# Optimization experiments

Hardware: AMD Instinct MI355X
Metric: run time of the kernel (lower is better)

## Reference

```python
import jax, jax.numpy as jnp
from jax import lax
import numpy as np

TOP_PERCENT = 1.3
KSIZE = 3
SIGMA = 0.3 * ((KSIZE - 1) * 0.5 - 1) + 0.8  # torchvision default sigma for ksize=3 -> 0.8


def _gaussian_kernel1d():
    x = jnp.arange(KSIZE, dtype=jnp.float32) - (KSIZE - 1) / 2.0
    k = jnp.exp(-0.5 * (x / SIGMA) ** 2)
    return k / k.sum()


def setup_inputs() -> dict:
    key = jax.random.key(0)
    img = jax.random.uniform(key, (3, 4096, 4096), dtype=jnp.float32)
    return {"img": img}


def reference(img):
    # --- rgb_to_grayscale (ITU-R 601 coefficients, as torchvision) ---
    gray = 0.2989 * img[0] + 0.587 * img[1] + 0.114 * img[2]  # [H, W]

    # --- separable 3x3 gaussian blur, reflect padding (torchvision) ---
    k = _gaussian_kernel1d()
    p = jnp.pad(gray, 1, mode="reflect")  # [H+2, W+2]
    # horizontal pass
    h = k[0] * p[:, :-2] + k[1] * p[:, 1:-1] + k[2] * p[:, 2:]  # [H+2, W]
    # vertical pass
    blur = k[0] * h[:-2, :] + k[1] * h[1:-1, :] + k[2] * h[2:, :]  # [H, W]

    # --- quantile threshold (linear interpolation, matches torch.quantile) ---
    q = (100.0 - TOP_PERCENT) / 100.0
    threshold = jnp.quantile(blur, q)
    mask = (blur >= threshold).astype(jnp.int32)  # [H, W]

    # --- binary opening with 5x5 ones footprint ---
    # erosion = min filter; outside-image treated as 0 (scipy border_value=0),
    # so pad explicitly with zeros and reduce with VALID windows.
    INT_MAX = np.iinfo(np.int32).max
    INT_MIN = np.iinfo(np.int32).min
    padded = jnp.pad(mask, 2)  # zero pad -> borders erode
    eroded = lax.reduce_window(padded, INT_MAX, lax.min, (5, 5), (1, 1), "VALID")
    # dilation = max filter; identity padding (-inf equiv) matches border_value=0
    opened = lax.reduce_window(eroded, INT_MIN, lax.max, (5, 5), (1, 1), "SAME")

    return opened[None, :, :].astype(jnp.int32)  # [1, H, W]
```

## Files before the change

kernel.cpp:

```cpp
#include <hip/hip_runtime.h>
#include <stdint.h>
#include <cmath>


#define HH 4096
#define WW 4096
#define KRANK 16559111u
#define CAP 65536u

__device__ __forceinline__ unsigned ukey(float v) {
  return (unsigned)(v * 268435456.0f);
}
__device__ __forceinline__ int refl(int i) {
  return i < 0 ? -i : (i > 4095 ? 8190 - i : i);
}
__device__ __forceinline__ float grayf(float r, float g, float b) {
  return __fadd_rn(__fadd_rn(__fmul_rn(0.2989f, r), __fmul_rn(0.587f, g)),
                   __fmul_rn(0.114f, b));
}
__device__ __forceinline__ float tap3(float a, float b, float c, float kn0, float kn1) {
  return __fadd_rn(__fadd_rn(__fmul_rn(kn0, a), __fmul_rn(kn1, b)),
                   __fmul_rn(kn0, c));
}

__global__ __launch_bounds__(256) void k_blur(const float* __restrict__ img,
    float4* __restrict__ blur4, unsigned* __restrict__ hist1,
    float kn0, float kn1) {
  __shared__ unsigned hist[4096];
  const int tid = threadIdx.x;
  for (int i = tid; i < 4096; i += 256) hist[i] = 0u;
  __syncthreads();

  const int lane = tid & 63, wv = tid >> 6;
  const int bc = (blockIdx.x & 15) << 8;
  const int r0 = (blockIdx.x >> 4) << 6;
  const int rstart = r0 + (wv << 4);
  const float* __restrict__ Rp = img;
  const float* __restrict__ Gp = img + 16777216;
  const float* __restrict__ Bp = img + 33554432;
  const int c4 = bc + (lane << 2);

  auto hrow = [&](int r) -> float4 {
    const int gr = refl(r);
    const size_t base = ((size_t)gr << 12) + c4;
    float4 R = *(const float4*)(Rp + base);
    float4 G = *(const float4*)(Gp + base);
    float4 B = *(const float4*)(Bp + base);
    float4 g;
    g.x = grayf(R.x, G.x, B.x);
    g.y = grayf(R.y, G.y, B.y);
    g.z = grayf(R.z, G.z, B.z);
    g.w = grayf(R.w, G.w, B.w);
    float gl = __shfl_up(g.w, 1);
    float gr_ = __shfl_down(g.x, 1);
    if (lane == 0) {
      if (bc == 0) gl = g.y;
      else {
        size_t o = ((size_t)gr << 12) + bc - 1;
        gl = grayf(Rp[o], Gp[o], Bp[o]);
      }
    }
    if (lane == 63) {
      if (bc == 3840) gr_ = g.z;
      else {
        size_t o = ((size_t)gr << 12) + bc + 256;
        gr_ = grayf(Rp[o], Gp[o], Bp[o]);
      }
    }
    float4 h;
    h.x = tap3(gl, g.x, g.y, kn0, kn1);
    h.y = tap3(g.x, g.y, g.z, kn0, kn1);
    h.z = tap3(g.y, g.z, g.w, kn0, kn1);
    h.w = tap3(g.z, g.w, gr_, kn0, kn1);
    return h;
  };

  float4 h0 = hrow(rstart - 1);
  float4 h1 = hrow(rstart);
  for (int i = 0; i < 16; ++i) {
    float4 h2 = hrow(rstart + 1 + i);
    float4 v;
    v.x = tap3(h0.x, h1.x, h2.x, kn0, kn1);
    v.y = tap3(h0.y, h1.y, h2.y, kn0, kn1);
    v.z = tap3(h0.z, h1.z, h2.z, kn0, kn1);
    v.w = tap3(h0.w, h1.w, h2.w, kn0, kn1);
    blur4[(((size_t)(rstart + i) << 12) + c4) >> 2] = v;
    atomicAdd(&hist[ukey(v.x) >> 16], 1u);
    atomicAdd(&hist[ukey(v.y) >> 16], 1u);
    atomicAdd(&hist[ukey(v.z) >> 16], 1u);
    atomicAdd(&hist[ukey(v.w) >> 16], 1u);
    h0 = h1; h1 = h2;
  }
  __syncthreads();
  for (int i = tid; i < 4096; i += 256) {
    unsigned c = hist[i];
    if (c) atomicAdd(&hist1[i], c);
  }
}

__global__ __launch_bounds__(256) void k_sel1(const unsigned* __restrict__ hist1,
                                              unsigned* __restrict__ sel) {
  __shared__ unsigned part[256];
  const int t = threadIdx.x;
  unsigned loc[16];
  unsigned s = 0;
  for (int i = 0; i < 16; ++i) { loc[i] = hist1[t * 16 + i]; s += loc[i]; }
  part[t] = s;
  __syncthreads();
  for (int off = 1; off < 256; off <<= 1) {
    unsigned v = (t >= off) ? part[t - off] : 0u;
    __syncthreads();
    part[t] += v;
    __syncthreads();
  }
  unsigned incl = part[t], excl = incl - s;
  if (excl <= KRANK && KRANK < incl) {
    unsigned p = excl;
    for (int i = 0; i < 16; ++i) {
      if (KRANK < p + loc[i]) { sel[0] = (unsigned)(t * 16 + i); sel[1] = KRANK - p; break; }
      p += loc[i];
    }
  }
}

__global__ __launch_bounds__(256) void k_pass2(const float* __restrict__ blur,
    const unsigned* __restrict__ sel, unsigned* __restrict__ hist2,
    unsigned* __restrict__ cnt, unsigned long long* __restrict__ list,
    unsigned long long* __restrict__ mbits) {
  const unsigned b1 = sel[0];
  const unsigned ub = (b1 + 1u) << 16;
  unsigned i = blockIdx.x * 256 + threadIdx.x;
  unsigned u = ukey(blur[i]);
  unsigned long long w = __ballot(u >= ub);
  if ((threadIdx.x & 63) == 0) mbits[i >> 6] = w;
  if ((u >> 16) == b1) {
    atomicAdd(&hist2[u & 0xFFFFu], 1u);
    unsigned idx = atomicAdd(cnt, 1u);
    if (idx < CAP) list[idx] = ((unsigned long long)i << 16) | (u & 0xFFFFu);
  }
}

__global__ __launch_bounds__(1024) void k_sel2(const unsigned* __restrict__ hist2,
                                               unsigned* __restrict__ sel) {
  __shared__ unsigned part[1024];
  const int t = threadIdx.x;
  const unsigned base = (unsigned)t * 64u;
  unsigned s = 0;
  for (int i = 0; i < 64; ++i) s += hist2[base + i];
  part[t] = s;
  __syncthreads();
  for (int off = 1; off < 1024; off <<= 1) {
    unsigned v = (t >= off) ? part[t - off] : 0u;
    __syncthreads();
    part[t] += v;
    __syncthreads();
  }
  unsigned incl = part[t], excl = incl - s;
  unsigned r1 = sel[1];
  if (excl <= r1 && r1 < incl) {
    unsigned p = excl;
    for (int i = 0; i < 64; ++i) {
      unsigned c = hist2[base + i];
      if (r1 < p + c) { sel[2] = base + i; break; }
      p += c;
    }
  }
}

__global__ __launch_bounds__(256) void k_fixup(
    const unsigned long long* __restrict__ list, const unsigned* __restrict__ cnt,
    const unsigned* __restrict__ sel, unsigned long long* __restrict__ mbits) {
  unsigned n = *cnt; if (n > CAP) n = CAP;
  const unsigned lo = sel[2];
  for (unsigned j = blockIdx.x * 256 + threadIdx.x; j < n; j += 256 * gridDim.x) {
    unsigned long long e = list[j];
    if ((unsigned)(e & 0xFFFFu) >= lo) {
      unsigned long long pix = e >> 16;
      atomicOr(&mbits[pix >> 6], 1ull << (pix & 63));
    }
  }
}

__global__ __launch_bounds__(256) void k_erode(
    const unsigned long long* __restrict__ mbits,
    unsigned long long* __restrict__ ebits) {
  int w = blockIdx.x * 256 + threadIdx.x;
  int r = w >> 6, wc = w & 63;
  unsigned long long acc = ~0ull;
  for (int dr = -2; dr <= 2; ++dr) {
    int rr = r + dr;
    unsigned long long h = 0ull;
    if (rr >= 0 && rr <= HH - 1) {
      int rb = (rr << 6) + wc;
      unsigned long long C = mbits[rb];
      unsigned long long L = (wc > 0) ? mbits[rb - 1] : 0ull;
      unsigned long long R = (wc < 63) ? mbits[rb + 1] : 0ull;
      h = C & ((C >> 1) | (R << 63)) & ((C >> 2) | (R << 62))
            & ((C << 1) | (L >> 63)) & ((C << 2) | (L >> 62));
    }
    acc &= h;
  }
  ebits[w] = acc;
}

__global__ __launch_bounds__(256) void k_dilate_out(
    const unsigned long long* __restrict__ ebits, int4* __restrict__ out4) {
  __shared__ unsigned long long wbuf[256];
  int w = blockIdx.x * 256 + threadIdx.x;
  int r = w >> 6, wc = w & 63;
  unsigned long long acc = 0ull;
  for (int dr = -2; dr <= 2; ++dr) {
    int rr = r + dr;
    if (rr < 0 || rr > HH - 1) continue;
    int rb = (rr << 6) + wc;
    unsigned long long C = ebits[rb];
    unsigned long long L = (wc > 0) ? ebits[rb - 1] : 0ull;
    unsigned long long R = (wc < 63) ? ebits[rb + 1] : 0ull;
    acc |= C | ((C >> 1) | (R << 63)) | ((C >> 2) | (R << 62))
             | ((C << 1) | (L >> 63)) | ((C << 2) | (L >> 62));
  }
  wbuf[threadIdx.x] = acc;
  __syncthreads();
  size_t p0 = (size_t)blockIdx.x * 4096;
  for (int j = threadIdx.x; j < 4096; j += 256) {
    unsigned long long word = wbuf[j >> 4];
    unsigned nib = (unsigned)(word >> ((j & 15) << 2)) & 0xFu;
    out4[p0 + j] = make_int4(nib & 1, (nib >> 1) & 1, (nib >> 2) & 1, (nib >> 3) & 1);
  }
}

extern "C" void kernel_launch(void* const* d_in, const int* in_sizes, int n_in,
                              void* d_out, int out_size, void* d_ws, size_t ws_size,
                              hipStream_t stream) {
  (void)in_sizes; (void)n_in; (void)out_size; (void)ws_size;
  const float* img = (const float*)d_in[0];
  char* ws = (char*)d_ws;

  float* blur = (float*)ws;
  unsigned* hist1 = (unsigned*)(ws + 67108864);
  unsigned* hist2 = (unsigned*)(ws + 67125248);
  unsigned* cnt   = (unsigned*)(ws + 67387392);
  unsigned* sel   = (unsigned*)(ws + 67387456);
  unsigned long long* list  = (unsigned long long*)(ws + 67387520);
  unsigned long long* mbits = (unsigned long long*)(ws + 67911808);
  unsigned long long* ebits = (unsigned long long*)(ws + 70008960);

  float t = 1.0f / 0.8f;
  float k0 = expf(-0.5f * (t * t));
  float k1 = 1.0f;
  float s = (k0 + k1) + k0;
  float kn0 = k0 / s, kn1 = k1 / s;

  hipMemsetAsync(hist1, 0, 16384 + 262144 + 64, stream);
  k_blur<<<1024, 256, 0, stream>>>(img, (float4*)blur, hist1, kn0, kn1);
  k_sel1<<<1, 256, 0, stream>>>(hist1, sel);
  k_pass2<<<65536, 256, 0, stream>>>(blur, sel, hist2, cnt, list, mbits);
  k_sel2<<<1, 1024, 0, stream>>>(hist2, sel);
  k_fixup<<<32, 256, 0, stream>>>(list, cnt, sel, mbits);
  k_erode<<<1024, 256, 0, stream>>>(mbits, ebits);
  k_dilate_out<<<1024, 256, 0, stream>>>(ebits, (int4*)d_out);
}
```

Before: 371.5 us.

## Fuse erode/dilate, merge select with fixup, batch pass2 appends

```diff
diff --git a/kernel.cpp b/kernel.cpp
--- a/kernel.cpp
+++ b/kernel.cpp
@@ -23,50 +23,43 @@
                    __fmul_rn(kn0, c));
 }
 
-__global__ __launch_bounds__(256) void k_blur(const float* __restrict__ img,
+__global__ __launch_bounds__(512) void k_blur(const float* __restrict__ img,
     float4* __restrict__ blur4, unsigned* __restrict__ hist1,
     float kn0, float kn1) {
   __shared__ unsigned hist[4096];
   const int tid = threadIdx.x;
-  for (int i = tid; i < 4096; i += 256) hist[i] = 0u;
+  #pragma unroll
+  for (int i = tid; i < 4096; i += 512) hist[i] = 0u;
   __syncthreads();
 
   const int lane = tid & 63, wv = tid >> 6;
   const int bc = (blockIdx.x & 15) << 8;
   const int r0 = (blockIdx.x >> 4) << 6;
-  const int rstart = r0 + (wv << 4);
+  const int rstart = r0 + (wv << 3);
   const float* __restrict__ Rp = img;
   const float* __restrict__ Gp = img + 16777216;
   const float* __restrict__ Bp = img + 33554432;
   const int c4 = bc + (lane << 2);
+  const int colL = (bc == 0) ? 1 : bc - 1;
+  const int colR = (bc == 3840) ? 4094 : bc + 256;
+  const int hc = (lane == 0) ? colL : ((lane == 63) ? colR : c4);
 
   auto hrow = [&](int r) -> float4 {
-    const int gr = refl(r);
-    const size_t base = ((size_t)gr << 12) + c4;
-    float4 R = *(const float4*)(Rp + base);
-    float4 G = *(const float4*)(Gp + base);
-    float4 B = *(const float4*)(Bp + base);
+    const size_t base = ((size_t)refl(r) << 12);
+    float4 R = *(const float4*)(Rp + base + c4);
+    float4 G = *(const float4*)(Gp + base + c4);
+    float4 B = *(const float4*)(Bp + base + c4);
+    float hr = Rp[base + hc], hg = Gp[base + hc], hb = Bp[base + hc];
     float4 g;
     g.x = grayf(R.x, G.x, B.x);
     g.y = grayf(R.y, G.y, B.y);
     g.z = grayf(R.z, G.z, B.z);
     g.w = grayf(R.w, G.w, B.w);
+    float ghalo = grayf(hr, hg, hb);
     float gl = __shfl_up(g.w, 1);
     float gr_ = __shfl_down(g.x, 1);
-    if (lane == 0) {
-      if (bc == 0) gl = g.y;
-      else {
-        size_t o = ((size_t)gr << 12) + bc - 1;
-        gl = grayf(Rp[o], Gp[o], Bp[o]);
-      }
-    }
-    if (lane == 63) {
-      if (bc == 3840) gr_ = g.z;
-      else {
-        size_t o = ((size_t)gr << 12) + bc + 256;
-        gr_ = grayf(Rp[o], Gp[o], Bp[o]);
-      }
-    }
+    gl = (lane == 0) ? ghalo : gl;
+    gr_ = (lane == 63) ? ghalo : gr_;
     float4 h;
     h.x = tap3(gl, g.x, g.y, kn0, kn1);
     h.y = tap3(g.x, g.y, g.z, kn0, kn1);
@@ -77,7 +70,8 @@
 
   float4 h0 = hrow(rstart - 1);
   float4 h1 = hrow(rstart);
-  for (int i = 0; i < 16; ++i) {
+  #pragma unroll
+  for (int i = 0; i < 8; ++i) {
     float4 h2 = hrow(rstart + 1 + i);
     float4 v;
     v.x = tap3(h0.x, h1.x, h2.x, kn0, kn1);
@@ -92,7 +86,8 @@
     h0 = h1; h1 = h2;
   }
   __syncthreads();
-  for (int i = tid; i < 4096; i += 256) {
+  #pragma unroll
+  for (int i = tid; i < 4096; i += 512) {
     unsigned c = hist[i];
     if (c) atomicAdd(&hist1[i], c);
   }
@@ -127,22 +122,47 @@
     const unsigned* __restrict__ sel, unsigned* __restrict__ hist2,
     unsigned* __restrict__ cnt, unsigned long long* __restrict__ list,
     unsigned long long* __restrict__ mbits) {
+  __shared__ unsigned lcnt, lbase;
+  __shared__ unsigned lidx[256];
+  __shared__ unsigned short lkey[256];
+  if (threadIdx.x == 0) lcnt = 0u;
+  __syncthreads();
   const unsigned b1 = sel[0];
   const unsigned ub = (b1 + 1u) << 16;
-  unsigned i = blockIdx.x * 256 + threadIdx.x;
-  unsigned u = ukey(blur[i]);
-  unsigned long long w = __ballot(u >= ub);
-  if ((threadIdx.x & 63) == 0) mbits[i >> 6] = w;
-  if ((u >> 16) == b1) {
-    atomicAdd(&hist2[u & 0xFFFFu], 1u);
-    unsigned idx = atomicAdd(cnt, 1u);
-    if (idx < CAP) list[idx] = ((unsigned long long)i << 16) | (u & 0xFFFFu);
-  }
-}
-
-__global__ __launch_bounds__(1024) void k_sel2(const unsigned* __restrict__ hist2,
-                                               unsigned* __restrict__ sel) {
+  const unsigned base = blockIdx.x * 8192u + threadIdx.x;
+  #pragma unroll 4
+  for (int it = 0; it < 32; ++it) {
+    unsigned i = base + (unsigned)it * 256u;
+    unsigned u = ukey(blur[i]);
+    unsigned long long w = __ballot(u >= ub);
+    if ((threadIdx.x & 63) == 0) mbits[i >> 6] = w;
+    if ((u >> 16) == b1) {
+      atomicAdd(&hist2[u & 0xFFFFu], 1u);
+      unsigned x = atomicAdd(&lcnt, 1u);
+      if (x < 256u) { lidx[x] = i; lkey[x] = (unsigned short)(u & 0xFFFFu); }
+      else {
+        unsigned g = atomicAdd(cnt, 1u);
+        if (g < CAP) list[g] = ((unsigned long long)i << 16) | (u & 0xFFFFu);
+      }
+    }
+  }
+  __syncthreads();
+  unsigned n = lcnt > 256u ? 256u : lcnt;
+  if (threadIdx.x == 0 && n) lbase = atomicAdd(cnt, n);
+  __syncthreads();
+  if (threadIdx.x < n) {
+    unsigned g = lbase + threadIdx.x;
+    if (g < CAP)
+      list[g] = ((unsigned long long)lidx[threadIdx.x] << 16) | (unsigned)lkey[threadIdx.x];
+  }
+}
+
+__global__ __launch_bounds__(1024) void k_sel2fix(const unsigned* __restrict__ hist2,
+    const unsigned* __restrict__ sel, const unsigned* __restrict__ cnt,
+    const unsigned long long* __restrict__ list,
+    unsigned long long* __restrict__ mbits) {
   __shared__ unsigned part[1024];
+  __shared__ unsigned sLo;
   const int t = threadIdx.x;
   const unsigned base = (unsigned)t * 64u;
   unsigned s = 0;
@@ -156,23 +176,19 @@
     __syncthreads();
   }
   unsigned incl = part[t], excl = incl - s;
-  unsigned r1 = sel[1];
+  const unsigned r1 = sel[1];
   if (excl <= r1 && r1 < incl) {
     unsigned p = excl;
     for (int i = 0; i < 64; ++i) {
       unsigned c = hist2[base + i];
-      if (r1 < p + c) { sel[2] = base + i; break; }
+      if (r1 < p + c) { sLo = base + i; break; }
       p += c;
     }
   }
-}
-
-__global__ __launch_bounds__(256) void k_fixup(
-    const unsigned long long* __restrict__ list, const unsigned* __restrict__ cnt,
-    const unsigned* __restrict__ sel, unsigned long long* __restrict__ mbits) {
+  __syncthreads();
+  const unsigned lo = sLo;
   unsigned n = *cnt; if (n > CAP) n = CAP;
-  const unsigned lo = sel[2];
-  for (unsigned j = blockIdx.x * 256 + threadIdx.x; j < n; j += 256 * gridDim.x) {
+  for (unsigned j = t; j < n; j += 1024) {
     unsigned long long e = list[j];
     if ((unsigned)(e & 0xFFFFu) >= lo) {
       unsigned long long pix = e >> 16;
@@ -181,49 +197,52 @@
   }
 }
 
-__global__ __launch_bounds__(256) void k_erode(
-    const unsigned long long* __restrict__ mbits,
-    unsigned long long* __restrict__ ebits) {
-  int w = blockIdx.x * 256 + threadIdx.x;
-  int r = w >> 6, wc = w & 63;
-  unsigned long long acc = ~0ull;
-  for (int dr = -2; dr <= 2; ++dr) {
-    int rr = r + dr;
-    unsigned long long h = 0ull;
-    if (rr >= 0 && rr <= HH - 1) {
-      int rb = (rr << 6) + wc;
-      unsigned long long C = mbits[rb];
-      unsigned long long L = (wc > 0) ? mbits[rb - 1] : 0ull;
-      unsigned long long R = (wc < 63) ? mbits[rb + 1] : 0ull;
-      h = C & ((C >> 1) | (R << 63)) & ((C >> 2) | (R << 62))
-            & ((C << 1) | (L >> 63)) & ((C << 2) | (L >> 62));
-    }
-    acc &= h;
-  }
-  ebits[w] = acc;
-}
-
-__global__ __launch_bounds__(256) void k_dilate_out(
-    const unsigned long long* __restrict__ ebits, int4* __restrict__ out4) {
-  __shared__ unsigned long long wbuf[256];
-  int w = blockIdx.x * 256 + threadIdx.x;
-  int r = w >> 6, wc = w & 63;
-  unsigned long long acc = 0ull;
-  for (int dr = -2; dr <= 2; ++dr) {
-    int rr = r + dr;
-    if (rr < 0 || rr > HH - 1) continue;
-    int rb = (rr << 6) + wc;
-    unsigned long long C = ebits[rb];
-    unsigned long long L = (wc > 0) ? ebits[rb - 1] : 0ull;
-    unsigned long long R = (wc < 63) ? ebits[rb + 1] : 0ull;
-    acc |= C | ((C >> 1) | (R << 63)) | ((C >> 2) | (R << 62))
-             | ((C << 1) | (L >> 63)) | ((C << 2) | (L >> 62));
-  }
-  wbuf[threadIdx.x] = acc;
-  __syncthreads();
-  size_t p0 = (size_t)blockIdx.x * 4096;
-  for (int j = threadIdx.x; j < 4096; j += 256) {
-    unsigned long long word = wbuf[j >> 4];
+__global__ __launch_bounds__(256) void k_morph(
+    const unsigned long long* __restrict__ mbits, int4* __restrict__ out4) {
+  __shared__ unsigned long long er[12][64];
+  __shared__ unsigned long long dl[8][64];
+  const int r0 = blockIdx.x << 3;
+  for (int t = threadIdx.x; t < 12 * 64; t += 256) {
+    int lr = t >> 6, wc = t & 63;
+    int rr = r0 - 2 + lr;
+    unsigned long long acc = 0ull;
+    if (rr >= 0 && rr < HH) {
+      acc = ~0ull;
+      #pragma unroll
+      for (int dr = -2; dr <= 2; ++dr) {
+        int mr = rr + dr;
+        unsigned long long h = 0ull;
+        if (mr >= 0 && mr < HH) {
+          int rb = (mr << 6) + wc;
+          unsigned long long C = mbits[rb];
+          unsigned long long L = (wc > 0) ? mbits[rb - 1] : 0ull;
+          unsigned long long R = (wc < 63) ? mbits[rb + 1] : 0ull;
+          h = C & ((C >> 1) | (R << 63)) & ((C >> 2) | (R << 62))
+                & ((C << 1) | (L >> 63)) & ((C << 2) | (L >> 62));
+        }
+        acc &= h;
+      }
+    }
+    er[lr][wc] = acc;
+  }
+  __syncthreads();
+  for (int t = threadIdx.x; t < 8 * 64; t += 256) {
+    int lr = t >> 6, wc = t & 63;
+    unsigned long long acc = 0ull;
+    #pragma unroll
+    for (int dr = 0; dr <= 4; ++dr) {
+      unsigned long long C = er[lr + dr][wc];
+      unsigned long long L = (wc > 0) ? er[lr + dr][wc - 1] : 0ull;
+      unsigned long long R = (wc < 63) ? er[lr + dr][wc + 1] : 0ull;
+      acc |= C | ((C >> 1) | (R << 63)) | ((C >> 2) | (R << 62))
+               | ((C << 1) | (L >> 63)) | ((C << 2) | (L >> 62));
+    }
+    dl[lr][wc] = acc;
+  }
+  __syncthreads();
+  const size_t p0 = (size_t)r0 << 10;
+  for (int j = threadIdx.x; j < 8192; j += 256) {
+    unsigned long long word = dl[j >> 10][(j >> 4) & 63];
     unsigned nib = (unsigned)(word >> ((j & 15) << 2)) & 0xFu;
     out4[p0 + j] = make_int4(nib & 1, (nib >> 1) & 1, (nib >> 2) & 1, (nib >> 3) & 1);
   }
@@ -243,7 +262,6 @@
   unsigned* sel   = (unsigned*)(ws + 67387456);
   unsigned long long* list  = (unsigned long long*)(ws + 67387520);
   unsigned long long* mbits = (unsigned long long*)(ws + 67911808);
-  unsigned long long* ebits = (unsigned long long*)(ws + 70008960);
 
   float t = 1.0f / 0.8f;
   float k0 = expf(-0.5f * (t * t));
@@ -252,11 +270,9 @@
   float kn0 = k0 / s, kn1 = k1 / s;
 
   hipMemsetAsync(hist1, 0, 16384 + 262144 + 64, stream);
-  k_blur<<<1024, 256, 0, stream>>>(img, (float4*)blur, hist1, kn0, kn1);
+  k_blur<<<1024, 512, 0, stream>>>(img, (float4*)blur, hist1, kn0, kn1);
   k_sel1<<<1, 256, 0, stream>>>(hist1, sel);
-  k_pass2<<<65536, 256, 0, stream>>>(blur, sel, hist2, cnt, list, mbits);
-  k_sel2<<<1, 1024, 0, stream>>>(hist2, sel);
-  k_fixup<<<32, 256, 0, stream>>>(list, cnt, sel, mbits);
-  k_erode<<<1024, 256, 0, stream>>>(mbits, ebits);
-  k_dilate_out<<<1024, 256, 0, stream>>>(ebits, (int4*)d_out);
-}
+  k_pass2<<<2048, 256, 0, stream>>>(blur, sel, hist2, cnt, list, mbits);
+  k_sel2fix<<<1, 1024, 0, stream>>>(hist2, sel, cnt, list, mbits);
+  k_morph<<<512, 256, 0, stream>>>(mbits, (int4*)d_out);
+}
```

Measured after the change: 365.7 us. Within noise of the previous version (-1.5%).
